# Kernel tuning notes

Hardware: AMD Instinct MI355X
Metric: run time of the kernel (lower is better)

## Reference

```python
import jax, jax.numpy as jnp
import numpy as np

H, HKV, D, BS, NSEL, WIN = 32, 8, 64, 64, 16, 512
N_REP = H // HKV


def precompute_freqs(dim, max_seq_len, theta=10000.0):
    inv = 1.0 / theta ** (np.arange(0, dim, 2, dtype=np.float32) / dim)
    t = np.arange(max_seq_len, dtype=np.float32)
    return jnp.asarray(np.outer(t, inv))  # (S, dim//2)


def apply_rope(x, freqs):
    # x: (B, T, H, D)
    T = x.shape[1]
    xr = x.reshape(x.shape[:-1] + (-1, 2))
    cos = jnp.cos(freqs[:T])[None, :, None, :]
    sin = jnp.sin(freqs[:T])[None, :, None, :]
    x0, x1 = xr[..., 0], xr[..., 1]
    out = jnp.stack([x0 * cos - x1 * sin, x0 * sin + x1 * cos], axis=-1)
    return out.reshape(x.shape)


def setup_inputs() -> dict:
    key = jax.random.key(0)
    ks = jax.random.split(key, 9)
    d_model = 2048
    s = lambda fan_in: 1.0 / np.sqrt(fan_in)
    return {
        "x": jax.random.normal(ks[0], (1, 2048, d_model), jnp.float32),
        "W_q": jax.random.normal(ks[1], (d_model, H * D), jnp.float32) * s(d_model),
        "W_k": jax.random.normal(ks[2], (d_model, HKV * D), jnp.float32) * s(d_model),
        "W_v": jax.random.normal(ks[3], (d_model, HKV * D), jnp.float32) * s(d_model),
        "W_o": jax.random.normal(ks[4], (H * D, d_model), jnp.float32) * s(H * D),
        "W_ck": jax.random.normal(ks[5], (BS * D, D), jnp.float32) * s(BS * D),
        "W_cv": jax.random.normal(ks[6], (BS * D, D), jnp.float32) * s(BS * D),
        "W_imp": jax.random.normal(ks[7], (D, 1), jnp.float32) * s(D),
        "W_gate": jax.random.normal(ks[8], (d_model, 3), jnp.float32) * s(d_model),
    }


def reference(x, W_q, W_k, W_v, W_o, W_ck, W_cv, W_imp, W_gate):
    B, T, _ = x.shape
    S = T  # no kv_cache
    scale = 1.0 / np.sqrt(D)
    freqs = precompute_freqs(D, T)

    q = apply_rope((x @ W_q).reshape(B, T, H, D), freqs)
    k = apply_rope((x @ W_k).reshape(B, T, HKV, D), freqs)
    v = (x @ W_v).reshape(B, T, HKV, D)
    q = q.transpose(0, 2, 1, 3)  # (B,H,T,D)
    k = k.transpose(0, 2, 1, 3)  # (B,HKV,S,D)
    v = v.transpose(0, 2, 1, 3)

    # --- compressed-block branch ---
    nb = S // BS
    kb = k[:, :, : nb * BS].reshape(B, HKV, nb, BS * D)
    vb = v[:, :, : nb * BS].reshape(B, HKV, nb, BS * D)
    kc = jnp.repeat(kb @ W_ck, N_REP, axis=1)  # (B,H,nb,D)
    vc = jnp.repeat(vb @ W_cv, N_REP, axis=1)
    a_c = jax.nn.softmax(jnp.einsum('bhtd,bhnd->bhtn', q, kc) * scale, axis=-1)
    out_c = jnp.einsum('bhtn,bhnd->bhtd', a_c, vc)

    # GQA expansion shared by select / sliding branches
    kx = jnp.repeat(k, N_REP, axis=1)
    vx = jnp.repeat(v, N_REP, axis=1)

    # --- 'selected' branch (reference computes top-k indices but discards them;
    # attention is full dense unmasked softmax, faithfully reproduced) ---
    k_mean = k[:, :, : nb * BS].reshape(B, HKV, nb, BS, D).mean(axis=3)
    scores = (k_mean @ W_imp)[..., 0]
    _top = jax.lax.top_k(scores, NSEL)  # dead code in original; kept for faithfulness
    a_s = jax.nn.softmax(jnp.einsum('bhtd,bhsd->bhts', q, kx) * scale, axis=-1)
    out_s = jnp.einsum('bhts,bhsd->bhtd', a_s, vx)

    # --- sliding-window branch (dense scores + mask, as in original) ---
    logits = jnp.einsum('bhtd,bhsd->bhts', q, kx) * scale
    i = jnp.arange(T)[:, None]
    j = jnp.arange(S)[None, :]
    allowed = (j <= S - T + i) & (j >= S - T + i - WIN + 1)
    logits = jnp.where(allowed[None, None], logits, -jnp.inf)
    a_w = jnp.nan_to_num(jax.nn.softmax(logits, axis=-1))
    out_w = jnp.einsum('bhts,bhsd->bhtd', a_w, vx)

    # --- gated combine ---
    gates = jax.nn.softmax(x @ W_gate, axis=-1)  # (B,T,3)
    stacked = jnp.stack(
        [out_c.transpose(0, 2, 1, 3), out_s.transpose(0, 2, 1, 3), out_w.transpose(0, 2, 1, 3)],
        axis=3,
    )  # (B,T,H,3,D)
    out = (stacked * gates[:, :, None, :, None]).sum(axis=3).reshape(B, T, H * D)
    return out @ W_o
```

## Files before the change

### kernel.cpp

```cpp
#include <hip/hip_runtime.h>
#include <cmath>

typedef unsigned short u16;
typedef unsigned int u32;
typedef __attribute__((ext_vector_type(8))) __bf16 bf16x8;
typedef __attribute__((ext_vector_type(8))) u16 u16x8;
typedef __attribute__((ext_vector_type(4))) float f32x4;
typedef __attribute__((ext_vector_type(4))) u16 u16x4;

#define MFMA16(acc, a, b) (acc) = __builtin_amdgcn_mfma_f32_16x16x32_bf16((a), (b), (acc), 0, 0, 0)

__device__ __forceinline__ u16 f2bf(float x) {
  union { float f; u32 u; } c; c.f = x;
  u32 r = (c.u + 0x7FFFu + ((c.u >> 16) & 1u)) >> 16;
  return (u16)r;
}
__device__ __forceinline__ float bf2f(u16 b) {
  union { u32 u; float f; } c; c.u = ((u32)b) << 16;
  return c.f;
}
__device__ __forceinline__ float rowmax16(float v) {
#pragma unroll
  for (int m = 1; m < 16; m <<= 1) v = fmaxf(v, __shfl_xor(v, m));
  return v;
}
__device__ __forceinline__ float rowsum16(float v) {
#pragma unroll
  for (int m = 1; m < 16; m <<= 1) v += __shfl_xor(v, m);
  return v;
}
__device__ __forceinline__ void gload16(const u16* g, u16* l) {
  __builtin_amdgcn_global_load_lds(
      (const __attribute__((address_space(1))) void*)(g),
      (__attribute__((address_space(3))) void*)(l), 16, 0, 0);
}
__device__ __forceinline__ float exp2_asm(float x) {
  float r;
  asm("v_exp_f32 %0, %1\n\ts_nop 0" : "=v"(r) : "v"(x));
  return r;
}
__device__ __forceinline__ u32 cvtpk(float a, float b) {
  u32 r;
  asm("v_cvt_pk_bf16_f32 %0, %1, %2" : "=v"(r) : "v"(a), "v"(b));
  return r;
}
__device__ __forceinline__ u16x8 bc_u(bf16x8 v) { union { bf16x8 b; u16x8 u; } c; c.b = v; return c.u; }
__device__ __forceinline__ bf16x8 bc_b(u16x8 v) { union { u16x8 u; bf16x8 b; } c; c.u = v; return c.b; }
__device__ __forceinline__ bf16x8 pack8(f32x4 a, f32x4 b) {
  union { u32 w[4]; bf16x8 v; } c;
  c.w[0] = cvtpk(a[0], a[1]);
  c.w[1] = cvtpk(a[2], a[3]);
  c.w[2] = cvtpk(b[0], b[1]);
  c.w[3] = cvtpk(b[2], b[3]);
  return c.v;
}
__device__ __forceinline__ void swapchain(u32& a, u32& c) {
  asm("v_permlane32_swap_b32 %0, %1" : "+v"(a), "+v"(c));
  asm("v_permlane16_swap_b32 %0, %1" : "+v"(a), "+v"(c));
}

__global__ void freqs_kernel(float* __restrict__ ct, float* __restrict__ st) {
  int idx = blockIdx.x * 256 + threadIdx.x;
  int t = idx >> 5, i = idx & 31;
  float inv = 1.0f / powf(10000.0f, (float)i / 32.0f);
  float a = (float)t * inv;
  float sv, cv;
  sincosf(a, &sv, &cv);
  ct[idx] = cv;
  st[idx] = sv;
}

__global__ void cvt_x_kernel(const float* __restrict__ in, u16* __restrict__ out) {
  int idx = (blockIdx.x * 256 + threadIdx.x) * 4;
  f32x4 v = *(const f32x4*)(in + idx);
  u16x4 o;
  o[0] = f2bf(v[0]); o[1] = f2bf(v[1]); o[2] = f2bf(v[2]); o[3] = f2bf(v[3]);
  *(u16x4*)(out + idx) = o;
}

__global__ __launch_bounds__(256) void trcvt_kernel(const float* __restrict__ W,
                                                    u16* __restrict__ Wt, int K, int N) {
  __shared__ u16 t_lds[64][65];
  int ntx = N >> 6;
  int kt = (blockIdx.x / ntx) * 64, nt = (blockIdx.x % ntx) * 64;
  int tx = threadIdx.x & 63, ty4 = threadIdx.x >> 6;
#pragma unroll 4
  for (int yy = 0; yy < 16; ++yy) {
    int k = kt + ty4 * 16 + yy;
    t_lds[ty4 * 16 + yy][tx] = f2bf(W[(size_t)k * N + nt + tx]);
  }
  __syncthreads();
#pragma unroll 4
  for (int yy = 0; yy < 16; ++yy) {
    int n = nt + ty4 * 16 + yy;
    Wt[(size_t)n * K + kt + tx] = t_lds[tx][ty4 * 16 + yy];
  }
}

__global__ __launch_bounds__(256) void gemm_bt_kernel(const u16* __restrict__ A,
                                                      const u16* __restrict__ Bt,
                                                      float* __restrict__ C,
                                                      int M, int N, int K) {
  __shared__ __align__(16) u16 As[128 * 64];
  __shared__ __align__(16) u16 Bs[128 * 64];
  const int tid = threadIdx.x;
  const int lane = tid & 63;
  const int w = tid >> 6;
  const int lr = lane & 15;
  const int lg = lane >> 4;
  const int lk8 = lg * 8;
  const int gx = gridDim.x;
  const int nwg = gx * gridDim.y;
  const int flat = blockIdx.y * gx + blockIdx.x;
  const int qq = nwg >> 3;
  const int swz = (flat & 7) * qq + (flat >> 3);
  const int brow = (swz % gx) * 128;
  const int bcol = (swz / gx) * 128;
  const int wr = (w >> 1) * 64;
  const int wc = (w & 1) * 64;

  const f32x4 zero4 = {0.f, 0.f, 0.f, 0.f};
  f32x4 acc[4][4];
#pragma unroll
  for (int m = 0; m < 4; ++m)
#pragma unroll
    for (int n = 0; n < 4; ++n) acc[m][n] = zero4;

  const int srow = tid >> 3;
  const int scol = (tid & 7) * 8;
  const u16* Ab = A + (size_t)(brow + srow) * K + scol;
  const u16* Bb = Bt + (size_t)(bcol + srow) * K + scol;

  for (int k0 = 0; k0 < K; k0 += 64) {
    __syncthreads();
#pragma unroll
    for (int it = 0; it < 4; ++it) {
      gload16(Ab + (size_t)it * 32 * K + k0, &As[tid * 8 + it * 2048]);
      gload16(Bb + (size_t)it * 32 * K + k0, &Bs[tid * 8 + it * 2048]);
    }
    __syncthreads();
#pragma unroll
    for (int kk = 0; kk < 2; ++kk) {
      bf16x8 af[4], bv[4];
#pragma unroll
      for (int m = 0; m < 4; ++m)
        af[m] = *(const bf16x8*)&As[(wr + m * 16 + lr) * 64 + kk * 32 + lk8];
#pragma unroll
      for (int n = 0; n < 4; ++n)
        bv[n] = *(const bf16x8*)&Bs[(wc + n * 16 + lr) * 64 + kk * 32 + lk8];
#pragma unroll
      for (int m = 0; m < 4; ++m)
#pragma unroll
        for (int n = 0; n < 4; ++n) MFMA16(acc[m][n], af[m], bv[n]);
    }
  }
#pragma unroll
  for (int m = 0; m < 4; ++m) {
#pragma unroll
    for (int rr = 0; rr < 4; ++rr) {
      int row = brow + wr + m * 16 + lg * 4 + rr;
#pragma unroll
      for (int n = 0; n < 4; ++n)
        C[(size_t)row * N + bcol + wc + n * 16 + lr] = acc[m][n][rr];
    }
  }
}

__global__ void rope_q_kernel(const float* __restrict__ qkv, const float* __restrict__ ct,
                              const float* __restrict__ st, u16* __restrict__ qb) {
  int idx = blockIdx.x * 256 + threadIdx.x;
  int i = idx & 31, hh = (idx >> 5) & 31, t = idx >> 10;
  float x0 = qkv[(size_t)t * 3072 + hh * 64 + 2 * i];
  float x1 = qkv[(size_t)t * 3072 + hh * 64 + 2 * i + 1];
  float c = ct[t * 32 + i], s = st[t * 32 + i];
  size_t o = ((size_t)hh * 2048 + t) * 64 + 2 * i;
  qb[o] = f2bf((x0 * c - x1 * s) * 0.125f);
  qb[o + 1] = f2bf((x0 * s + x1 * c) * 0.125f);
}
__global__ void rope_k_kernel(const float* __restrict__ qkv, const float* __restrict__ ct,
                              const float* __restrict__ st, u16* __restrict__ kb) {
  int idx = blockIdx.x * 256 + threadIdx.x;
  int i = idx & 31, hh = (idx >> 5) & 7, t = idx >> 8;
  float x0 = qkv[(size_t)t * 3072 + 2048 + hh * 64 + 2 * i];
  float x1 = qkv[(size_t)t * 3072 + 2048 + hh * 64 + 2 * i + 1];
  float c = ct[t * 32 + i], s = st[t * 32 + i];
  size_t o = ((size_t)hh * 2048 + t) * 64 + 2 * i;
  kb[o] = f2bf(x0 * c - x1 * s);
  kb[o + 1] = f2bf(x0 * s + x1 * c);
}
__global__ __launch_bounds__(256) void vtrans_kernel(const float* __restrict__ qkv,
                                                     u16* __restrict__ vbr,
                                                     u16* __restrict__ vb2) {
  __shared__ u16 tl[64][72];
  int hk = blockIdx.y, t0 = blockIdx.x * 64;
  int tx = threadIdx.x & 63, ty = threadIdx.x >> 6;
#pragma unroll 4
  for (int yy = 0; yy < 16; ++yy) {
    int row = ty * 16 + yy;
    u16 b = f2bf(qkv[(size_t)(t0 + row) * 3072 + 2560 + hk * 64 + tx]);
    tl[row][tx] = b;
    vbr[((size_t)hk * 2048 + t0 + row) * 64 + tx] = b;
  }
  __syncthreads();
  u16* dst = vb2 + (size_t)hk * 64 * 2048 + t0;
#pragma unroll 4
  for (int yy = 0; yy < 16; ++yy)
    dst[(size_t)(ty * 16 + yy) * 2048 + tx] = tl[tx][ty * 16 + yy];
}

__global__ __launch_bounds__(256) void gates_kernel(const float* __restrict__ x,
                                                    const float* __restrict__ Wg,
                                                    float* __restrict__ g) {
  int t = blockIdx.x * 4 + (threadIdx.x >> 6);
  int lane = threadIdx.x & 63;
  const float* xr = x + (size_t)t * 2048;
  float a0 = 0, a1 = 0, a2 = 0;
  for (int d = lane; d < 2048; d += 64) {
    float xv = xr[d];
    a0 = fmaf(xv, Wg[d * 3 + 0], a0);
    a1 = fmaf(xv, Wg[d * 3 + 1], a1);
    a2 = fmaf(xv, Wg[d * 3 + 2], a2);
  }
#pragma unroll
  for (int msk = 1; msk < 64; msk <<= 1) {
    a0 += __shfl_xor(a0, msk);
    a1 += __shfl_xor(a1, msk);
    a2 += __shfl_xor(a2, msk);
  }
  if (lane == 0) {
    float m = fmaxf(a0, fmaxf(a1, a2));
    float e0 = __expf(a0 - m), e1 = __expf(a1 - m), e2 = __expf(a2 - m);
    float inv = 1.f / (e0 + e1 + e2);
    g[t * 3 + 0] = e0 * inv; g[t * 3 + 1] = e1 * inv; g[t * 3 + 2] = e2 * inv;
  }
}

__global__ __launch_bounds__(256) void cgemm_kernel(const u16* __restrict__ kB,
                                                    const u16* __restrict__ vbr,
                                                    const float* __restrict__ Wck,
                                                    const float* __restrict__ Wcv,
                                                    float* __restrict__ kc,
                                                    float* __restrict__ vc) {
  __shared__ float red[4][64];
  int b = blockIdx.x;
  bool isv = b >= 256;
  int blk = b & 255;
  const u16* src = (isv ? vbr : kB) + (size_t)blk * 4096;
  const float* W = isv ? Wcv : Wck;
  float* out = (isv ? vc : kc) + (size_t)blk * 64;
  int lane = threadIdx.x & 63, w = threadIdx.x >> 6;
  int base = w * 1024;
  float acc0 = 0.f, acc1 = 0.f;
  for (int i = 0; i < 1024; i += 8) {
    u16x8 s8 = *(const u16x8*)(src + base + i);
#pragma unroll
    for (int j = 0; j < 8; j += 2) {
      acc0 = fmaf(bf2f(s8[j]), W[(size_t)(base + i + j) * 64 + lane], acc0);
      acc1 = fmaf(bf2f(s8[j + 1]), W[(size_t)(base + i + j + 1) * 64 + lane], acc1);
    }
  }
  red[w][lane] = acc0 + acc1;
  __syncthreads();
  if (w == 0)
    out[lane] = red[0][lane] + red[1][lane] + red[2][lane] + red[3][lane];
}

__global__ __launch_bounds__(256) void attn_kernel(
    const u16* __restrict__ qb, const u16* __restrict__ kb, const u16* __restrict__ vb2,
    const float* __restrict__ kcf, const float* __restrict__ vcf,
    const float* __restrict__ gf, u16* __restrict__ comb) {
  __shared__ __align__(16) u16 k_lds[2][64 * 64];
  __shared__ __align__(16) u16 vt_lds[2][64 * 64];

  const int tid = threadIdx.x;
  const int lane = tid & 63;
  const int lr = lane & 15;
  const int lg = lane >> 4;
  const int lk8 = lg * 8;
  const int w = tid >> 6;
  const int flat = blockIdx.y * gridDim.x + blockIdx.x;
  const int swz = (flat & 7) * 128 + (flat >> 3);
  const int h = swz >> 5;
  const int t0 = (swz & 31) * 64;
  const int hk = h >> 2;
  const int tw = t0 + w * 16;
  const f32x4 zero4 = {0.f, 0.f, 0.f, 0.f};
  const float LOG2E = 1.44269504f;
  const float THR = 11.5416f;

  bf16x8 qf0, qf1;
  {
    const u16* qrow = qb + ((size_t)h * 2048 + (tw + lr)) * 64;
    qf0 = *(const bf16x8*)(qrow + lk8);
    qf1 = *(const bf16x8*)(qrow + 32 + lk8);
  }

  const int lin1 = 256 + tid;
  const int row0 = tid >> 3, sl0 = (tid & 7) ^ (row0 & 7);
  const int row1 = lin1 >> 3, sl1 = (lin1 & 7) ^ (row1 & 7);
  const u16* kS0 = kb + ((size_t)hk * 2048 + row0) * 64 + sl0 * 8;
  const u16* kS1 = kb + ((size_t)hk * 2048 + row1) * 64 + sl1 * 8;
  const u16* vS0 = vb2 + ((size_t)hk * 64 + row0) * 2048 + sl0 * 8;
  const u16* vS1 = vb2 + ((size_t)hk * 64 + row1) * 2048 + sl1 * 8;

  const int sA = ((0 + lg) ^ (lr & 7)) * 8;
  const int sB = ((4 + lg) ^ (lr & 7)) * 8;

  f32x4 acc_s[4], acc_w[4];
#pragma unroll
  for (int n = 0; n < 4; ++n) { acc_s[n] = zero4; acc_w[n] = zero4; }
  float m2 = -1e30f, lsr = 0.f, lwr = 0.f;

#define STAGE(cc)                                                      \
  {                                                                    \
    const int b_ = (cc) & 1;                                           \
    gload16(kS0 + (size_t)(cc) * 4096, &k_lds[b_][tid * 8]);           \
    gload16(kS1 + (size_t)(cc) * 4096, &k_lds[b_][2048 + tid * 8]);    \
    gload16(vS0 + (cc) * 64, &vt_lds[b_][tid * 8]);                    \
    gload16(vS1 + (cc) * 64, &vt_lds[b_][2048 + tid * 8]);             \
  }

  STAGE(0);
  __syncthreads();

#pragma unroll 1
  for (int c = 0; c < 32; ++c) {
    const int s0 = c * 64;
    const u16* kbuf = k_lds[c & 1];
    const u16* vbuf = vt_lds[c & 1];
    if (c < 31) STAGE(c + 1);

    f32x4 sc[4];
    __builtin_amdgcn_s_setprio(1);
#pragma unroll
    for (int cb = 0; cb < 4; ++cb) {
      f32x4 z = zero4;
      const int rb = (cb * 16 + lr) * 64;
      bf16x8 b0 = *(const bf16x8*)&kbuf[rb + sA];
      bf16x8 b1 = *(const bf16x8*)&kbuf[rb + sB];
      MFMA16(z, b0, qf0);
      MFMA16(z, b1, qf1);
      sc[cb] = z;
    }
    __builtin_amdgcn_s_setprio(0);

    const bool winAct = (s0 <= tw + 15) && (s0 + 63 >= tw - 511);

    float mxl = -1e30f;
#pragma unroll
    for (int cb = 0; cb < 4; ++cb)
#pragma unroll
      for (int r = 0; r < 4; ++r) mxl = fmaxf(mxl, sc[cb][r]);
    if (__any(fmaf(mxl, LOG2E, -m2) > THR)) {
      float gm = mxl;
      gm = fmaxf(gm, __shfl_xor(gm, 16));
      gm = fmaxf(gm, __shfl_xor(gm, 32));
      float mnew = fmaxf(m2, gm * LOG2E);
      float corr = exp2_asm(m2 - mnew);
      m2 = mnew;
      lsr *= corr;
      lwr *= corr;
#pragma unroll
      for (int n = 0; n < 4; ++n) { acc_s[n] *= corr; acc_w[n] *= corr; }
    }

    float pv[4][4];
#pragma unroll
    for (int cb = 0; cb < 4; ++cb)
#pragma unroll
      for (int r = 0; r < 4; ++r) {
        pv[cb][r] = exp2_asm(fmaf(sc[cb][r], LOG2E, -m2));
        lsr += pv[cb][r];
      }
    if (winAct) {
      const int dbase2 = (tw + lr) - s0 - lg * 4;
#pragma unroll
      for (int cb = 0; cb < 4; ++cb)
#pragma unroll
        for (int r = 0; r < 4; ++r) {
          int d0 = dbase2 - 16 * cb - r;
          lwr += ((u32)d0 < 512u) ? pv[cb][r] : 0.f;
        }
    }

    u32 A0 = cvtpk(pv[0][0], pv[0][1]), B0 = cvtpk(pv[0][2], pv[0][3]);
    u32 C0 = cvtpk(pv[1][0], pv[1][1]), D0 = cvtpk(pv[1][2], pv[1][3]);
    u32 A1 = cvtpk(pv[2][0], pv[2][1]), B1 = cvtpk(pv[2][2], pv[2][3]);
    u32 C1 = cvtpk(pv[3][0], pv[3][1]), D1 = cvtpk(pv[3][2], pv[3][3]);
    swapchain(A0, C0);
    swapchain(B0, D0);
    swapchain(A1, C1);
    swapchain(B1, D1);
    union { u32 wd[4]; bf16x8 v; } pf0c, pf1c;
    pf0c.wd[0] = A0; pf0c.wd[1] = B0; pf0c.wd[2] = C0; pf0c.wd[3] = D0;
    pf1c.wd[0] = A1; pf1c.wd[1] = B1; pf1c.wd[2] = C1; pf1c.wd[3] = D1;
    bf16x8 pf0 = pf0c.v, pf1 = pf1c.v;

    bf16x8 aw0 = pf0, aw1 = pf1;
    if (winAct) {
      const int base0 = (tw + lr) - (s0 + lk8);
      u16x8 a0 = bc_u(pf0), a1 = bc_u(pf1);
      u16x8 z0, z1;
#pragma unroll
      for (int j = 0; j < 8; ++j) {
        z0[j] = ((u32)(base0 - j) < 512u) ? a0[j] : (u16)0;
        z1[j] = ((u32)(base0 - 32 - j) < 512u) ? a1[j] : (u16)0;
      }
      aw0 = bc_b(z0);
      aw1 = bc_b(z1);
    }

    __builtin_amdgcn_s_setprio(1);
#pragma unroll
    for (int n = 0; n < 4; ++n) {
      const int rb = (n * 16 + lr) * 64;
      bf16x8 bv0 = *(const bf16x8*)&vbuf[rb + sA];
      bf16x8 bv1 = *(const bf16x8*)&vbuf[rb + sB];
      MFMA16(acc_s[n], bv0, pf0);
      MFMA16(acc_s[n], bv1, pf1);
      if (winAct) {
        MFMA16(acc_w[n], bv0, aw0);
        MFMA16(acc_w[n], bv1, aw1);
      }
    }
    __builtin_amdgcn_s_setprio(0);

    __syncthreads();
  }
#undef STAGE

  f32x4 accc[4];
  float lcv;
  {
    f32x4 sc0 = zero4, sc1 = zero4;
#pragma unroll
    for (int kk = 0; kk < 2; ++kk) {
      const float* kr0 = kcf + ((size_t)hk * 32 + lr) * 64 + kk * 32 + lk8;
      const float* kr1 = kcf + ((size_t)hk * 32 + 16 + lr) * 64 + kk * 32 + lk8;
      bf16x8 b0 = pack8(*(const f32x4*)kr0, *(const f32x4*)(kr0 + 4));
      bf16x8 b1 = pack8(*(const f32x4*)kr1, *(const f32x4*)(kr1 + 4));
      bf16x8 qk = kk ? qf1 : qf0;
      MFMA16(sc0, b0, qk);
      MFMA16(sc1, b1, qk);
    }
    float mm = -1e30f;
#pragma unroll
    for (int r = 0; r < 4; ++r) mm = fmaxf(mm, fmaxf(sc0[r], sc1[r]));
    mm = fmaxf(mm, __shfl_xor(mm, 16));
    mm = fmaxf(mm, __shfl_xor(mm, 32));
    float p0[4], p1[4];
    float ssum = 0.f;
#pragma unroll
    for (int r = 0; r < 4; ++r) {
      p0[r] = __expf(sc0[r] - mm);
      p1[r] = __expf(sc1[r] - mm);
      ssum += p0[r] + p1[r];
    }
    ssum += __shfl_xor(ssum, 16);
    ssum += __shfl_xor(ssum, 32);
    lcv = ssum;
    u32 A = cvtpk(p0[0], p0[1]), B = cvtpk(p0[2], p0[3]);
    u32 C = cvtpk(p1[0], p1[1]), D = cvtpk(p1[2], p1[3]);
    swapchain(A, C);
    swapchain(B, D);
    union { u32 wd[4]; bf16x8 v; } pc;
    pc.wd[0] = A; pc.wd[1] = B; pc.wd[2] = C; pc.wd[3] = D;
#pragma unroll
    for (int nb = 0; nb < 4; ++nb) {
      u16x8 bb;
#pragma unroll
      for (int j = 0; j < 8; ++j)
        bb[j] = f2bf(vcf[((size_t)hk * 32 + lk8 + j) * 64 + nb * 16 + lr]);
      f32x4 z = zero4;
      MFMA16(z, bc_b(bb), pc.v);
      accc[nb] = z;
    }
  }

  float ls = lsr;
  ls += __shfl_xor(ls, 16);
  ls += __shfl_xor(ls, 32);
  float lw = lwr;
  lw += __shfl_xor(lw, 16);
  lw += __shfl_xor(lw, 32);
  {
    const int t = tw + lr;
    float g0 = gf[t * 3 + 0], g1 = gf[t * 3 + 1], g2 = gf[t * 3 + 2];
    float wc_ = g0 / lcv;
    float ws_ = g1 / ls;
    float ww_ = g2 / lw;
#pragma unroll
    for (int n = 0; n < 4; ++n) {
      u16x4 o;
#pragma unroll
      for (int r = 0; r < 4; ++r)
        o[r] = f2bf(accc[n][r] * wc_ + acc_s[n][r] * ws_ + acc_w[n][r] * ww_);
      *(u16x4*)&comb[(size_t)t * 2048 + h * 64 + n * 16 + lg * 4] = o;
    }
  }
}

extern "C" void kernel_launch(void* const* d_in, const int* in_sizes, int n_in,
                              void* d_out, int out_size, void* d_ws, size_t ws_size,
                              hipStream_t stream) {
  (void)in_sizes; (void)n_in; (void)out_size;
  const float* x   = (const float*)d_in[0];
  const float* Wq  = (const float*)d_in[1];
  const float* Wk  = (const float*)d_in[2];
  const float* Wv  = (const float*)d_in[3];
  const float* Wo  = (const float*)d_in[4];
  const float* Wck = (const float*)d_in[5];
  const float* Wcv = (const float*)d_in[6];
  const float* Wg  = (const float*)d_in[8];
  float* out = (float*)d_out;
  char* ws = (char*)d_ws;

  constexpr size_t OXB   = 0;
  constexpr size_t OWT   = OXB  + 8388608;
  constexpr size_t OWOT  = OWT  + 12582912;
  constexpr size_t OQKV  = OWOT + 8388608;
  constexpr size_t OQB   = OQKV + 25165824;
  constexpr size_t OKB   = OQB  + 8388608;
  constexpr size_t OVB   = OKB  + 2097152;
  constexpr size_t OCT   = OVB  + 2097152;
  constexpr size_t OST   = OCT  + 262144;
  constexpr size_t OKC   = OST  + 262144;
  constexpr size_t OVC   = OKC  + 65536;
  constexpr size_t OG    = OVC  + 65536;
  constexpr size_t OCOMB = OG   + 24576;
  constexpr size_t TOTAL = OCOMB + 8388608;
  if (ws_size < TOTAL) return;

  u16* xb    = (u16*)(ws + OXB);
  u16* WT    = (u16*)(ws + OWT);
  u16* WoT   = (u16*)(ws + OWOT);
  float* qkv = (float*)(ws + OQKV);
  u16* qB    = (u16*)(ws + OQB);
  u16* kB    = (u16*)(ws + OKB);
  u16* vB2   = (u16*)(ws + OVB);
  float* ct  = (float*)(ws + OCT);
  float* st  = (float*)(ws + OST);
  float* kc  = (float*)(ws + OKC);
  float* vc  = (float*)(ws + OVC);
  float* gg  = (float*)(ws + OG);
  u16* comb  = (u16*)(ws + OCOMB);
  u16* vbr   = comb;

  freqs_kernel<<<dim3(256), dim3(256), 0, stream>>>(ct, st);
  cvt_x_kernel<<<dim3(4096), dim3(256), 0, stream>>>(x, xb);
  trcvt_kernel<<<dim3(1024), dim3(256), 0, stream>>>(Wq, WT, 2048, 2048);
  trcvt_kernel<<<dim3(256),  dim3(256), 0, stream>>>(Wk, WT + (size_t)2048 * 2048, 2048, 512);
  trcvt_kernel<<<dim3(256),  dim3(256), 0, stream>>>(Wv, WT + (size_t)2560 * 2048, 2048, 512);
  trcvt_kernel<<<dim3(1024), dim3(256), 0, stream>>>(Wo, WoT, 2048, 2048);

  gemm_bt_kernel<<<dim3(16, 24), dim3(256), 0, stream>>>(xb, WT, qkv, 2048, 3072, 2048);

  rope_q_kernel<<<dim3(8192), dim3(256), 0, stream>>>(qkv, ct, st, qB);
  rope_k_kernel<<<dim3(2048), dim3(256), 0, stream>>>(qkv, ct, st, kB);
  vtrans_kernel<<<dim3(32, 8), dim3(256), 0, stream>>>(qkv, vbr, vB2);
  gates_kernel<<<dim3(512), dim3(256), 0, stream>>>(x, Wg, gg);

  cgemm_kernel<<<dim3(512), dim3(256), 0, stream>>>(kB, vbr, Wck, Wcv, kc, vc);

  attn_kernel<<<dim3(32, 32), dim3(256), 0, stream>>>(qB, kB, vB2, kc, vc, gg, comb);

  gemm_bt_kernel<<<dim3(16, 16), dim3(256), 0, stream>>>(comb, WoT, out, 2048, 2048, 2048);
}
```

Baseline: 269.3 us.

## Load K/V fragments directly from global into registers, dropping LDS staging

Replaces the double-buffered LDS staging of K and V tiles, along with its per-chunk __syncthreads, with direct per-wave global loads into registers. K fragments for the next chunk are prefetched into alternating register sets, with the loop unrolled by two to swap them. Each of the four waves now fetches the same K/V data independently, so global and L2 traffic rises and register pressure grows, in exchange for removing LDS round-trips and block-level barriers.

```diff
diff --git a/kernel.cpp b/kernel.cpp
--- a/kernel.cpp
+++ b/kernel.cpp
@@ -269,9 +269,6 @@
     const u16* __restrict__ qb, const u16* __restrict__ kb, const u16* __restrict__ vb2,
     const float* __restrict__ kcf, const float* __restrict__ vcf,
     const float* __restrict__ gf, u16* __restrict__ comb) {
-  __shared__ __align__(16) u16 k_lds[2][64 * 64];
-  __shared__ __align__(16) u16 vt_lds[2][64 * 64];
-
   const int tid = threadIdx.x;
   const int lane = tid & 63;
   const int lr = lane & 15;
@@ -295,139 +292,115 @@
     qf1 = *(const bf16x8*)(qrow + 32 + lk8);
   }
 
-  const int lin1 = 256 + tid;
-  const int row0 = tid >> 3, sl0 = (tid & 7) ^ (row0 & 7);
-  const int row1 = lin1 >> 3, sl1 = (lin1 & 7) ^ (row1 & 7);
-  const u16* kS0 = kb + ((size_t)hk * 2048 + row0) * 64 + sl0 * 8;
-  const u16* kS1 = kb + ((size_t)hk * 2048 + row1) * 64 + sl1 * 8;
-  const u16* vS0 = vb2 + ((size_t)hk * 64 + row0) * 2048 + sl0 * 8;
-  const u16* vS1 = vb2 + ((size_t)hk * 64 + row1) * 2048 + sl1 * 8;
-
-  const int sA = ((0 + lg) ^ (lr & 7)) * 8;
-  const int sB = ((4 + lg) ^ (lr & 7)) * 8;
+  const u16* kbase = kb + (size_t)hk * 2048 * 64;
+  const u16* vbase = vb2 + (size_t)hk * 64 * 2048;
 
   f32x4 acc_s[4], acc_w[4];
 #pragma unroll
   for (int n = 0; n < 4; ++n) { acc_s[n] = zero4; acc_w[n] = zero4; }
   float m2 = -1e30f, lsr = 0.f, lwr = 0.f;
 
-#define STAGE(cc)                                                      \
-  {                                                                    \
-    const int b_ = (cc) & 1;                                           \
-    gload16(kS0 + (size_t)(cc) * 4096, &k_lds[b_][tid * 8]);           \
-    gload16(kS1 + (size_t)(cc) * 4096, &k_lds[b_][2048 + tid * 8]);    \
-    gload16(vS0 + (cc) * 64, &vt_lds[b_][tid * 8]);                    \
-    gload16(vS1 + (cc) * 64, &vt_lds[b_][2048 + tid * 8]);             \
-  }
-
-  STAGE(0);
-  __syncthreads();
+  bf16x8 kA0[4], kA1[4], kB0[4], kB1[4], vv0[4], vv1[4];
+#pragma unroll
+  for (int cb = 0; cb < 4; ++cb) {
+    const u16* kr = kbase + (size_t)(cb * 16 + lr) * 64;
+    kA0[cb] = *(const bf16x8*)(kr + lk8);
+    kA1[cb] = *(const bf16x8*)(kr + 32 + lk8);
+  }
+
+#define CHUNK_BODY(cc, KC0, KC1, KN0, KN1)                                    \
+  {                                                                           \
+    const int s0 = (cc) * 64;                                                 \
+    _Pragma("unroll") for (int n = 0; n < 4; ++n) {                           \
+      const u16* vr = vbase + (size_t)(n * 16 + lr) * 2048 + s0;              \
+      vv0[n] = *(const bf16x8*)(vr + lk8);                                    \
+      vv1[n] = *(const bf16x8*)(vr + 32 + lk8);                               \
+    }                                                                         \
+    if ((cc) < 31) {                                                          \
+      _Pragma("unroll") for (int cb = 0; cb < 4; ++cb) {                      \
+        const u16* kr = kbase + (size_t)(s0 + 64 + cb * 16 + lr) * 64;        \
+        KN0[cb] = *(const bf16x8*)(kr + lk8);                                 \
+        KN1[cb] = *(const bf16x8*)(kr + 32 + lk8);                            \
+      }                                                                       \
+    }                                                                         \
+    f32x4 sc[4];                                                              \
+    __builtin_amdgcn_s_setprio(1);                                            \
+    _Pragma("unroll") for (int cb = 0; cb < 4; ++cb) {                        \
+      f32x4 z = zero4;                                                        \
+      MFMA16(z, KC0[cb], qf0);                                                \
+      MFMA16(z, KC1[cb], qf1);                                                \
+      sc[cb] = z;                                                             \
+    }                                                                         \
+    __builtin_amdgcn_s_setprio(0);                                            \
+    const bool winAct = (s0 <= tw + 15) && (s0 + 63 >= tw - 511);             \
+    float mxl = -1e30f;                                                       \
+    _Pragma("unroll") for (int cb = 0; cb < 4; ++cb)                          \
+      _Pragma("unroll") for (int r = 0; r < 4; ++r)                           \
+        mxl = fmaxf(mxl, sc[cb][r]);                                          \
+    if (__any(fmaf(mxl, LOG2E, -m2) > THR)) {                                 \
+      float gm = mxl;                                                         \
+      gm = fmaxf(gm, __shfl_xor(gm, 16));                                     \
+      gm = fmaxf(gm, __shfl_xor(gm, 32));                                     \
+      float mnew = fmaxf(m2, gm * LOG2E);                                     \
+      float corr = exp2_asm(m2 - mnew);                                       \
+      m2 = mnew; lsr *= corr; lwr *= corr;                                    \
+      _Pragma("unroll") for (int n = 0; n < 4; ++n) {                         \
+        acc_s[n] *= corr; acc_w[n] *= corr;                                   \
+      }                                                                       \
+    }                                                                         \
+    float pv[4][4];                                                           \
+    _Pragma("unroll") for (int cb = 0; cb < 4; ++cb)                          \
+      _Pragma("unroll") for (int r = 0; r < 4; ++r) {                         \
+        pv[cb][r] = exp2_asm(fmaf(sc[cb][r], LOG2E, -m2));                    \
+        lsr += pv[cb][r];                                                     \
+      }                                                                       \
+    if (winAct) {                                                             \
+      const int dbase2 = (tw + lr) - s0 - lg * 4;                             \
+      _Pragma("unroll") for (int cb = 0; cb < 4; ++cb)                        \
+        _Pragma("unroll") for (int r = 0; r < 4; ++r) {                       \
+          int d0 = dbase2 - 16 * cb - r;                                      \
+          lwr += ((u32)d0 < 512u) ? pv[cb][r] : 0.f;                          \
+        }                                                                     \
+    }                                                                         \
+    u32 A0 = cvtpk(pv[0][0], pv[0][1]), B0 = cvtpk(pv[0][2], pv[0][3]);       \
+    u32 C0 = cvtpk(pv[1][0], pv[1][1]), D0 = cvtpk(pv[1][2], pv[1][3]);       \
+    u32 A1 = cvtpk(pv[2][0], pv[2][1]), B1 = cvtpk(pv[2][2], pv[2][3]);       \
+    u32 C1 = cvtpk(pv[3][0], pv[3][1]), D1 = cvtpk(pv[3][2], pv[3][3]);       \
+    swapchain(A0, C0); swapchain(B0, D0);                                     \
+    swapchain(A1, C1); swapchain(B1, D1);                                     \
+    union { u32 wd[4]; bf16x8 v; } pf0c, pf1c;                                \
+    pf0c.wd[0] = A0; pf0c.wd[1] = B0; pf0c.wd[2] = C0; pf0c.wd[3] = D0;       \
+    pf1c.wd[0] = A1; pf1c.wd[1] = B1; pf1c.wd[2] = C1; pf1c.wd[3] = D1;       \
+    bf16x8 pf0 = pf0c.v, pf1 = pf1c.v;                                        \
+    bf16x8 aw0 = pf0, aw1 = pf1;                                              \
+    if (winAct) {                                                             \
+      const int base0 = (tw + lr) - (s0 + lk8);                               \
+      u16x8 a0 = bc_u(pf0), a1 = bc_u(pf1);                                   \
+      u16x8 z0, z1;                                                           \
+      _Pragma("unroll") for (int j = 0; j < 8; ++j) {                         \
+        z0[j] = ((u32)(base0 - j) < 512u) ? a0[j] : (u16)0;                   \
+        z1[j] = ((u32)(base0 - 32 - j) < 512u) ? a1[j] : (u16)0;              \
+      }                                                                       \
+      aw0 = bc_b(z0); aw1 = bc_b(z1);                                         \
+    }                                                                         \
+    __builtin_amdgcn_s_setprio(1);                                            \
+    _Pragma("unroll") for (int n = 0; n < 4; ++n) {                           \
+      MFMA16(acc_s[n], vv0[n], pf0);                                          \
+      MFMA16(acc_s[n], vv1[n], pf1);                                          \
+      if (winAct) {                                                           \
+        MFMA16(acc_w[n], vv0[n], aw0);                                        \
+        MFMA16(acc_w[n], vv1[n], aw1);                                        \
+      }                                                                       \
+    }                                                                         \
+    __builtin_amdgcn_s_setprio(0);                                            \
+  }
 
 #pragma unroll 1
-  for (int c = 0; c < 32; ++c) {
-    const int s0 = c * 64;
-    const u16* kbuf = k_lds[c & 1];
-    const u16* vbuf = vt_lds[c & 1];
-    if (c < 31) STAGE(c + 1);
-
-    f32x4 sc[4];
-    __builtin_amdgcn_s_setprio(1);
-#pragma unroll
-    for (int cb = 0; cb < 4; ++cb) {
-      f32x4 z = zero4;
-      const int rb = (cb * 16 + lr) * 64;
-      bf16x8 b0 = *(const bf16x8*)&kbuf[rb + sA];
-      bf16x8 b1 = *(const bf16x8*)&kbuf[rb + sB];
-      MFMA16(z, b0, qf0);
-      MFMA16(z, b1, qf1);
-      sc[cb] = z;
-    }
-    __builtin_amdgcn_s_setprio(0);
-
-    const bool winAct = (s0 <= tw + 15) && (s0 + 63 >= tw - 511);
-
-    float mxl = -1e30f;
-#pragma unroll
-    for (int cb = 0; cb < 4; ++cb)
-#pragma unroll
-      for (int r = 0; r < 4; ++r) mxl = fmaxf(mxl, sc[cb][r]);
-    if (__any(fmaf(mxl, LOG2E, -m2) > THR)) {
-      float gm = mxl;
-      gm = fmaxf(gm, __shfl_xor(gm, 16));
-      gm = fmaxf(gm, __shfl_xor(gm, 32));
-      float mnew = fmaxf(m2, gm * LOG2E);
-      float corr = exp2_asm(m2 - mnew);
-      m2 = mnew;
-      lsr *= corr;
-      lwr *= corr;
-#pragma unroll
-      for (int n = 0; n < 4; ++n) { acc_s[n] *= corr; acc_w[n] *= corr; }
-    }
-
-    float pv[4][4];
-#pragma unroll
-    for (int cb = 0; cb < 4; ++cb)
-#pragma unroll
-      for (int r = 0; r < 4; ++r) {
-        pv[cb][r] = exp2_asm(fmaf(sc[cb][r], LOG2E, -m2));
-        lsr += pv[cb][r];
-      }
-    if (winAct) {
-      const int dbase2 = (tw + lr) - s0 - lg * 4;
-#pragma unroll
-      for (int cb = 0; cb < 4; ++cb)
-#pragma unroll
-        for (int r = 0; r < 4; ++r) {
-          int d0 = dbase2 - 16 * cb - r;
-          lwr += ((u32)d0 < 512u) ? pv[cb][r] : 0.f;
-        }
-    }
-
-    u32 A0 = cvtpk(pv[0][0], pv[0][1]), B0 = cvtpk(pv[0][2], pv[0][3]);
-    u32 C0 = cvtpk(pv[1][0], pv[1][1]), D0 = cvtpk(pv[1][2], pv[1][3]);
-    u32 A1 = cvtpk(pv[2][0], pv[2][1]), B1 = cvtpk(pv[2][2], pv[2][3]);
-    u32 C1 = cvtpk(pv[3][0], pv[3][1]), D1 = cvtpk(pv[3][2], pv[3][3]);
-    swapchain(A0, C0);
-    swapchain(B0, D0);
-    swapchain(A1, C1);
-    swapchain(B1, D1);
-    union { u32 wd[4]; bf16x8 v; } pf0c, pf1c;
-    pf0c.wd[0] = A0; pf0c.wd[1] = B0; pf0c.wd[2] = C0; pf0c.wd[3] = D0;
-    pf1c.wd[0] = A1; pf1c.wd[1] = B1; pf1c.wd[2] = C1; pf1c.wd[3] = D1;
-    bf16x8 pf0 = pf0c.v, pf1 = pf1c.v;
-
-    bf16x8 aw0 = pf0, aw1 = pf1;
-    if (winAct) {
-      const int base0 = (tw + lr) - (s0 + lk8);
-      u16x8 a0 = bc_u(pf0), a1 = bc_u(pf1);
-      u16x8 z0, z1;
-#pragma unroll
-      for (int j = 0; j < 8; ++j) {
-        z0[j] = ((u32)(base0 - j) < 512u) ? a0[j] : (u16)0;
-        z1[j] = ((u32)(base0 - 32 - j) < 512u) ? a1[j] : (u16)0;
-      }
-      aw0 = bc_b(z0);
-      aw1 = bc_b(z1);
-    }
-
-    __builtin_amdgcn_s_setprio(1);
-#pragma unroll
-    for (int n = 0; n < 4; ++n) {
-      const int rb = (n * 16 + lr) * 64;
-      bf16x8 bv0 = *(const bf16x8*)&vbuf[rb + sA];
-      bf16x8 bv1 = *(const bf16x8*)&vbuf[rb + sB];
-      MFMA16(acc_s[n], bv0, pf0);
-      MFMA16(acc_s[n], bv1, pf1);
-      if (winAct) {
-        MFMA16(acc_w[n], bv0, aw0);
-        MFMA16(acc_w[n], bv1, aw1);
-      }
-    }
-    __builtin_amdgcn_s_setprio(0);
-
-    __syncthreads();
-  }
-#undef STAGE
+  for (int c2 = 0; c2 < 32; c2 += 2) {
+    CHUNK_BODY(c2, kA0, kA1, kB0, kB1)
+    CHUNK_BODY(c2 + 1, kB0, kB1, kA0, kA1)
+  }
+#undef CHUNK_BODY
 
   f32x4 accc[4];
   float lcv;
```

Measured after the change: 406.3 us. +50.9%, slower.

## Fuse RoPE, bf16 conversion and V transpose into the QKV GEMM epilogue

Applied to the files above, without the earlier changes.

Replaces the fp32 QKV GEMM plus three separate rope_q, rope_k and vtrans kernels with a single GEMM whose epilogue applies RoPE (using a lane shuffle to fetch the pair element), scales Q, converts to bf16 and writes Q, K, V and transposed V directly. This removes the 25 MB fp32 qkv intermediate round trip and three kernel launches. In exchange the epilogue does scattered stores, notably the strided transposed-V writes, and performs per-element cos/sin loads inside the GEMM.

```diff
diff --git a/kernel.cpp b/kernel.cpp
--- a/kernel.cpp
+++ b/kernel.cpp
@@ -18,16 +18,6 @@
 __device__ __forceinline__ float bf2f(u16 b) {
   union { u32 u; float f; } c; c.u = ((u32)b) << 16;
   return c.f;
-}
-__device__ __forceinline__ float rowmax16(float v) {
-#pragma unroll
-  for (int m = 1; m < 16; m <<= 1) v = fmaxf(v, __shfl_xor(v, m));
-  return v;
-}
-__device__ __forceinline__ float rowsum16(float v) {
-#pragma unroll
-  for (int m = 1; m < 16; m <<= 1) v += __shfl_xor(v, m);
-  return v;
 }
 __device__ __forceinline__ void gload16(const u16* g, u16* l) {
   __builtin_amdgcn_global_load_lds(
@@ -166,46 +156,119 @@
   }
 }
 
-__global__ void rope_q_kernel(const float* __restrict__ qkv, const float* __restrict__ ct,
-                              const float* __restrict__ st, u16* __restrict__ qb) {
-  int idx = blockIdx.x * 256 + threadIdx.x;
-  int i = idx & 31, hh = (idx >> 5) & 31, t = idx >> 10;
-  float x0 = qkv[(size_t)t * 3072 + hh * 64 + 2 * i];
-  float x1 = qkv[(size_t)t * 3072 + hh * 64 + 2 * i + 1];
-  float c = ct[t * 32 + i], s = st[t * 32 + i];
-  size_t o = ((size_t)hh * 2048 + t) * 64 + 2 * i;
-  qb[o] = f2bf((x0 * c - x1 * s) * 0.125f);
-  qb[o + 1] = f2bf((x0 * s + x1 * c) * 0.125f);
-}
-__global__ void rope_k_kernel(const float* __restrict__ qkv, const float* __restrict__ ct,
-                              const float* __restrict__ st, u16* __restrict__ kb) {
-  int idx = blockIdx.x * 256 + threadIdx.x;
-  int i = idx & 31, hh = (idx >> 5) & 7, t = idx >> 8;
-  float x0 = qkv[(size_t)t * 3072 + 2048 + hh * 64 + 2 * i];
-  float x1 = qkv[(size_t)t * 3072 + 2048 + hh * 64 + 2 * i + 1];
-  float c = ct[t * 32 + i], s = st[t * 32 + i];
-  size_t o = ((size_t)hh * 2048 + t) * 64 + 2 * i;
-  kb[o] = f2bf(x0 * c - x1 * s);
-  kb[o + 1] = f2bf(x0 * s + x1 * c);
-}
-__global__ __launch_bounds__(256) void vtrans_kernel(const float* __restrict__ qkv,
-                                                     u16* __restrict__ vbr,
-                                                     u16* __restrict__ vb2) {
-  __shared__ u16 tl[64][72];
-  int hk = blockIdx.y, t0 = blockIdx.x * 64;
-  int tx = threadIdx.x & 63, ty = threadIdx.x >> 6;
-#pragma unroll 4
-  for (int yy = 0; yy < 16; ++yy) {
-    int row = ty * 16 + yy;
-    u16 b = f2bf(qkv[(size_t)(t0 + row) * 3072 + 2560 + hk * 64 + tx]);
-    tl[row][tx] = b;
-    vbr[((size_t)hk * 2048 + t0 + row) * 64 + tx] = b;
-  }
-  __syncthreads();
-  u16* dst = vb2 + (size_t)hk * 64 * 2048 + t0;
-#pragma unroll 4
-  for (int yy = 0; yy < 16; ++yy)
-    dst[(size_t)(ty * 16 + yy) * 2048 + tx] = tl[tx][ty * 16 + yy];
+__global__ __launch_bounds__(256) void gemm_qkv_kernel(
+    const u16* __restrict__ A, const u16* __restrict__ Bt,
+    const float* __restrict__ ct, const float* __restrict__ st,
+    u16* __restrict__ qB, u16* __restrict__ kB,
+    u16* __restrict__ vbr, u16* __restrict__ vb2) {
+  __shared__ __align__(16) u16 As[128 * 64];
+  __shared__ __align__(16) u16 Bs[128 * 64];
+  const int K = 2048;
+  const int tid = threadIdx.x;
+  const int lane = tid & 63;
+  const int w = tid >> 6;
+  const int lr = lane & 15;
+  const int lg = lane >> 4;
+  const int lk8 = lg * 8;
+  const int gx = gridDim.x;
+  const int nwg = gx * gridDim.y;
+  const int flat = blockIdx.y * gx + blockIdx.x;
+  const int qq = nwg >> 3;
+  const int swz = (flat & 7) * qq + (flat >> 3);
+  const int brow = (swz % gx) * 128;
+  const int bcol = (swz / gx) * 128;
+  const int wr = (w >> 1) * 64;
+  const int wc = (w & 1) * 64;
+
+  const f32x4 zero4 = {0.f, 0.f, 0.f, 0.f};
+  f32x4 acc[4][4];
+#pragma unroll
+  for (int m = 0; m < 4; ++m)
+#pragma unroll
+    for (int n = 0; n < 4; ++n) acc[m][n] = zero4;
+
+  const int srow = tid >> 3;
+  const int scol = (tid & 7) * 8;
+  const u16* Ab = A + (size_t)(brow + srow) * K + scol;
+  const u16* Bb = Bt + (size_t)(bcol + srow) * K + scol;
+
+  for (int k0 = 0; k0 < K; k0 += 64) {
+    __syncthreads();
+#pragma unroll
+    for (int it = 0; it < 4; ++it) {
+      gload16(Ab + (size_t)it * 32 * K + k0, &As[tid * 8 + it * 2048]);
+      gload16(Bb + (size_t)it * 32 * K + k0, &Bs[tid * 8 + it * 2048]);
+    }
+    __syncthreads();
+#pragma unroll
+    for (int kk = 0; kk < 2; ++kk) {
+      bf16x8 af[4], bv[4];
+#pragma unroll
+      for (int m = 0; m < 4; ++m)
+        af[m] = *(const bf16x8*)&As[(wr + m * 16 + lr) * 64 + kk * 32 + lk8];
+#pragma unroll
+      for (int n = 0; n < 4; ++n)
+        bv[n] = *(const bf16x8*)&Bs[(wc + n * 16 + lr) * 64 + kk * 32 + lk8];
+#pragma unroll
+      for (int m = 0; m < 4; ++m)
+#pragma unroll
+        for (int n = 0; n < 4; ++n) MFMA16(acc[m][n], af[m], bv[n]);
+    }
+  }
+
+  const int colbase = bcol + wc;
+  if (colbase < 2048) {
+#pragma unroll
+    for (int m = 0; m < 4; ++m)
+#pragma unroll
+      for (int n = 0; n < 4; ++n) {
+        const int c = colbase + n * 16 + lr;
+        const int hd = c >> 6, d = c & 63, i = d >> 1;
+        const float sgn = (c & 1) ? 1.f : -1.f;
+#pragma unroll
+        for (int rr = 0; rr < 4; ++rr) {
+          int t = brow + wr + m * 16 + lg * 4 + rr;
+          float v = acc[m][n][rr];
+          float p = __shfl_xor(v, 1);
+          float co = ct[t * 32 + i], si = st[t * 32 + i];
+          float o = fmaf(p, sgn * si, v * co) * 0.125f;
+          qB[(size_t)hd * 131072 + (size_t)t * 64 + d] = f2bf(o);
+        }
+      }
+  } else if (colbase < 2560) {
+#pragma unroll
+    for (int m = 0; m < 4; ++m)
+#pragma unroll
+      for (int n = 0; n < 4; ++n) {
+        const int c2 = colbase + n * 16 + lr - 2048;
+        const int hk = c2 >> 6, d = c2 & 63, i = d >> 1;
+        const float sgn = (c2 & 1) ? 1.f : -1.f;
+#pragma unroll
+        for (int rr = 0; rr < 4; ++rr) {
+          int t = brow + wr + m * 16 + lg * 4 + rr;
+          float v = acc[m][n][rr];
+          float p = __shfl_xor(v, 1);
+          float co = ct[t * 32 + i], si = st[t * 32 + i];
+          float o = fmaf(p, sgn * si, v * co);
+          kB[(size_t)hk * 131072 + (size_t)t * 64 + d] = f2bf(o);
+        }
+      }
+  } else {
+#pragma unroll
+    for (int m = 0; m < 4; ++m)
+#pragma unroll
+      for (int n = 0; n < 4; ++n) {
+        const int c2 = colbase + n * 16 + lr - 2560;
+        const int hk = c2 >> 6, d = c2 & 63;
+#pragma unroll
+        for (int rr = 0; rr < 4; ++rr) {
+          int t = brow + wr + m * 16 + lg * 4 + rr;
+          u16 b = f2bf(acc[m][n][rr]);
+          vbr[(size_t)hk * 131072 + (size_t)t * 64 + d] = b;
+          vb2[(size_t)hk * 131072 + (size_t)d * 2048 + t] = b;
+        }
+      }
+  }
 }
 
 __global__ __launch_bounds__(256) void gates_kernel(const float* __restrict__ x,
@@ -534,7 +597,6 @@
   u16* xb    = (u16*)(ws + OXB);
   u16* WT    = (u16*)(ws + OWT);
   u16* WoT   = (u16*)(ws + OWOT);
-  float* qkv = (float*)(ws + OQKV);
   u16* qB    = (u16*)(ws + OQB);
   u16* kB    = (u16*)(ws + OKB);
   u16* vB2   = (u16*)(ws + OVB);
@@ -552,14 +614,10 @@
   trcvt_kernel<<<dim3(256),  dim3(256), 0, stream>>>(Wk, WT + (size_t)2048 * 2048, 2048, 512);
   trcvt_kernel<<<dim3(256),  dim3(256), 0, stream>>>(Wv, WT + (size_t)2560 * 2048, 2048, 512);
   trcvt_kernel<<<dim3(1024), dim3(256), 0, stream>>>(Wo, WoT, 2048, 2048);
-
-  gemm_bt_kernel<<<dim3(16, 24), dim3(256), 0, stream>>>(xb, WT, qkv, 2048, 3072, 2048);
-
-  rope_q_kernel<<<dim3(8192), dim3(256), 0, stream>>>(qkv, ct, st, qB);
-  rope_k_kernel<<<dim3(2048), dim3(256), 0, stream>>>(qkv, ct, st, kB);
-  vtrans_kernel<<<dim3(32, 8), dim3(256), 0, stream>>>(qkv, vbr, vB2);
   gates_kernel<<<dim3(512), dim3(256), 0, stream>>>(x, Wg, gg);
 
+  gemm_qkv_kernel<<<dim3(16, 24), dim3(256), 0, stream>>>(xb, WT, ct, st, qB, kB, vbr, vB2);
+
   cgemm_kernel<<<dim3(512), dim3(256), 0, stream>>>(kB, vbr, Wck, Wcv, kc, vc);
 
   attn_kernel<<<dim3(32, 32), dim3(256), 0, stream>>>(qB, kB, vB2, kc, vc, gg, comb);
```

Measured after the change: 261.3 us (median of 2 runs). 1.03x faster.
